# Optimization experiments

Measured on AMD Instinct MI355X. Metric: run time of the kernel, lower is better.

The kernel has to match this reference:

```python
import jax, jax.numpy as jnp
import numpy as np

B, N, C = 4, 4096, 256
NUM_HEADS = 8
NUM_GROUPS = 4  # num_groups2, recursive_index=True path
HEAD_DIM = C // NUM_HEADS
SCALE = HEAD_DIM ** -0.5


def setup_inputs() -> dict:
    key = jax.random.key(0)
    k_x, k_idx, k_qkv, k_proj, k_pb = jax.random.split(key, 5)
    x = jax.random.normal(k_x, (B, N, C), dtype=jnp.float32)
    idx = jax.random.permutation(k_idx, N)  # random token shuffle (torch.randperm)
    # nn.Linear params (torch convention: y = x @ W.T + b)
    w_qkv = jax.random.normal(k_qkv, (3 * C, C), dtype=jnp.float32) * (1.0 / np.sqrt(C))
    w_proj = jax.random.normal(k_proj, (C, C), dtype=jnp.float32) * (1.0 / np.sqrt(C))
    b_proj = jax.random.normal(k_pb, (C,), dtype=jnp.float32) * 0.01
    return {"x": x, "idx": idx, "w_qkv": w_qkv, "w_proj": w_proj, "b_proj": b_proj}


def reference(x, idx, w_qkv, w_proj, b_proj):
    g, H, d = NUM_GROUPS, NUM_HEADS, HEAD_DIM
    n = N // g  # tokens per group
    inverse = jnp.argsort(idx)
    xp = x[:, idx, :]  # shuffled tokens [B, N, C]
    # qkv projection then split into groups/heads: [B, g, n, 3, H, d]
    qkv = (xp @ w_qkv.T).reshape(B, g, n, 3, H, d)
    q = qkv[:, :, :, 0].transpose(0, 1, 3, 2, 4)  # [B, g, H, n, d]
    k = qkv[:, :, :, 1].transpose(0, 1, 3, 2, 4)
    v = qkv[:, :, :, 2].transpose(0, 1, 3, 2, 4)
    attn = jnp.einsum('bghnd,bghmd->bghnm', q, k) * SCALE  # [B, g, H, n, n]
    attn = jax.nn.softmax(attn, axis=-1)
    o = jnp.einsum('bghnm,bghmd->bghnd', attn, v)
    # [B, g, H, n, d] -> [B, g, n, H, d] -> [B, N, C] (group-major token order)
    o = o.transpose(0, 1, 3, 2, 4).reshape(B, N, C)
    o = o[:, inverse, :]  # undo the shuffle
    return o @ w_proj.T + b_proj
```

## Files before the change

### kernel.cpp

```cpp
#include <hip/hip_runtime.h>
#include <hip/hip_bf16.h>


typedef __attribute__((ext_vector_type(8))) short bf16x8;
typedef __attribute__((ext_vector_type(4))) float f32x4;

__device__ __forceinline__ unsigned short f2bf(float x){
  __hip_bfloat16 h = __float2bfloat16(x);
  return __builtin_bit_cast(unsigned short, h);
}

__device__ __forceinline__ bf16x8 cvt8(const float4 f0, const float4 f1){
  bf16x8 v;
  v[0]=(short)f2bf(f0.x); v[1]=(short)f2bf(f0.y);
  v[2]=(short)f2bf(f0.z); v[3]=(short)f2bf(f0.w);
  v[4]=(short)f2bf(f1.x); v[5]=(short)f2bf(f1.y);
  v[6]=(short)f2bf(f1.z); v[7]=(short)f2bf(f1.w);
  return v;
}

#define QSCALE (0.17677669529663687f * 1.4426950408889634f)


__global__ __launch_bounds__(256, 3) void qkv_gemm(
    const float* __restrict__ x, const int* __restrict__ idx,
    const float* __restrict__ w_qkv,
    unsigned short* __restrict__ Qb, unsigned short* __restrict__ KF,
    unsigned short* __restrict__ VF)
{
  __shared__ __align__(16) unsigned short Asl[128*64];
  __shared__ __align__(16) unsigned short Bsl[128*64];
  const int tid = threadIdx.x;
  const int bid = blockIdx.x;
  const int u   = bid >> 3, xl = bid & 7;
  const int bx  = ((u & 15) << 3) + xl;
  const int by  = u >> 4;
  const int m0 = bx << 7;
  const int bb = bx >> 5;
  const int gg = (bx >> 3) & 3;
  const int j0 = (bx & 31) << 7;
  const int n0 = by << 7;

  int srow[2], brow[2], wb[2];
  #pragma unroll
  for (int it = 0; it < 2; ++it){
    int c = (it << 8) + tid;
    int row = c >> 2;
    int k8 = (c & 3) << 3;
    srow[it] = (bb << 12) + idx[j0 + row];
    brow[it] = n0 + row;
    wb[it] = ((row << 7) + (k8 << 1)) ^ ((row & 7) << 4);
  }

  #pragma unroll
  for (int it = 0; it < 2; ++it){
    int k8 = (((it << 8) + tid) & 3) << 3;
    const float* xs = x + srow[it]*256 + k8;
    const float* wsp = w_qkv + brow[it]*256 + k8;
    *(bf16x8*)((char*)Asl + wb[it]) = cvt8(*(const float4*)(xs), *(const float4*)(xs+4));
    *(bf16x8*)((char*)Bsl + wb[it]) = cvt8(*(const float4*)(wsp), *(const float4*)(wsp+4));
  }
  __syncthreads();

  const int lane = tid & 63;
  const int w = tid >> 6, wr = w >> 1, wc = w & 1;
  const int lr = lane & 15, lg = lane >> 4;
  const int ka = lg << 3;

  f32x4 acc[4][4];
  #pragma unroll
  for (int il = 0; il < 4; ++il)
    #pragma unroll
    for (int jl = 0; jl < 4; ++jl)
      acc[il][jl] = (f32x4){0.f,0.f,0.f,0.f};

  for (int st = 0; st < 8; ++st){
    float4 a0[2], a1[2], c0[2], c1[2];
    const bool pf = (st < 7);
    if (pf){
      int kb = (st + 1) << 5;
      #pragma unroll
      for (int it = 0; it < 2; ++it){
        int k8 = (((it << 8) + tid) & 3) << 3;
        const float* xs = x + srow[it]*256 + kb + k8;
        const float* wsp = w_qkv + brow[it]*256 + kb + k8;
        a0[it] = *(const float4*)(xs);  a1[it] = *(const float4*)(xs + 4);
        c0[it] = *(const float4*)(wsp); c1[it] = *(const float4*)(wsp + 4);
      }
    }

    bf16x8 af[4], bfr[4];
    #pragma unroll
    for (int il = 0; il < 4; ++il){
      int rowA = (wr << 6) + (il << 4) + lr;
      af[il] = *(const bf16x8*)((const char*)Asl + (((rowA << 7) + (ka << 1)) ^ ((rowA & 7) << 4)));
      int rowB = (wc << 6) + (il << 4) + lr;
      bfr[il] = *(const bf16x8*)((const char*)Bsl + (((rowB << 7) + (ka << 1)) ^ ((rowB & 7) << 4)));
    }
    __builtin_amdgcn_s_setprio(1);
    #pragma unroll
    for (int il = 0; il < 4; ++il)
      #pragma unroll
      for (int jl = 0; jl < 4; ++jl)
        acc[il][jl] = __builtin_amdgcn_mfma_f32_16x16x32_bf16(af[il], bfr[jl], acc[il][jl], 0, 0, 0);
    __builtin_amdgcn_s_setprio(0);

    __syncthreads();
    if (pf){
      #pragma unroll
      for (int it = 0; it < 2; ++it){
        *(bf16x8*)((char*)Asl + wb[it]) = cvt8(a0[it], a1[it]);
        *(bf16x8*)((char*)Bsl + wb[it]) = cvt8(c0[it], c1[it]);
      }
      __syncthreads();
    }
  }

  const int s = by >> 1;
  const int hbase = ((bb << 2) + gg) << 3;
  #pragma unroll
  for (int il = 0; il < 4; ++il){
    int mr0 = m0 + (wr << 6) + (il << 4) + (lg << 2);
    int nl0 = mr0 & 1023;
    int t   = nl0 >> 5;
    #pragma unroll
    for (int jl = 0; jl < 4; ++jl){
      int ocol = ((by & 1) << 7) + (wc << 6) + (jl << 4) + lr;
      int h  = ocol >> 5, dd = ocol & 31;
      int head = hbase + h;
      if (s == 2){
        int m = nl0 & 31;
        int lane2 = ((m >> 3) << 4) + (dd & 15);
        int half = dd >> 4;
        ushort4 pk;
        pk.x = f2bf(acc[il][jl][0]); pk.y = f2bf(acc[il][jl][1]);
        pk.z = f2bf(acc[il][jl][2]); pk.w = f2bf(acc[il][jl][3]);
        *(ushort4*)(VF + head*32768 + t*1024 + half*512 + lane2*8 + (m & 7)) = pk;
      } else if (s == 1){
        int r0 = nl0 & 31;
        int f  = (r0 >> 2) & 1;
        unsigned short* dst = KF + head*32768 + t*1024 + f*512
                             + ((((dd >> 3) << 4) + ((r0 >> 3) << 2)) << 3) + (dd & 7);
        dst[0]  = f2bf(acc[il][jl][0]);
        dst[8]  = f2bf(acc[il][jl][1]);
        dst[16] = f2bf(acc[il][jl][2]);
        dst[24] = f2bf(acc[il][jl][3]);
      } else {
        unsigned short* dst = Qb + head*32768 + dd;
        #pragma unroll
        for (int q = 0; q < 4; ++q)
          dst[(nl0 + q) << 5] = f2bf(acc[il][jl][q] * QSCALE);
      }
    }
  }
}

__device__ __forceinline__ void softmax16(
    const f32x4 s0, const f32x4 s1, const f32x4 s2, const f32x4 s3,
    bf16x8& pf0, bf16x8& pf1)
{
  float p0=__builtin_amdgcn_exp2f(s0[0]);  float p1=__builtin_amdgcn_exp2f(s0[1]);
  float p2=__builtin_amdgcn_exp2f(s0[2]);  float p3=__builtin_amdgcn_exp2f(s0[3]);
  float p4=__builtin_amdgcn_exp2f(s1[0]);  float p5=__builtin_amdgcn_exp2f(s1[1]);
  float p6=__builtin_amdgcn_exp2f(s1[2]);  float p7=__builtin_amdgcn_exp2f(s1[3]);
  float p8=__builtin_amdgcn_exp2f(s2[0]);  float p9=__builtin_amdgcn_exp2f(s2[1]);
  float p10=__builtin_amdgcn_exp2f(s2[2]); float p11=__builtin_amdgcn_exp2f(s2[3]);
  float p12=__builtin_amdgcn_exp2f(s3[0]); float p13=__builtin_amdgcn_exp2f(s3[1]);
  float p14=__builtin_amdgcn_exp2f(s3[2]); float p15=__builtin_amdgcn_exp2f(s3[3]);

  pf0[0]=(short)f2bf(p0);  pf0[1]=(short)f2bf(p1);
  pf0[2]=(short)f2bf(p2);  pf0[3]=(short)f2bf(p3);
  pf0[4]=(short)f2bf(p4);  pf0[5]=(short)f2bf(p5);
  pf0[6]=(short)f2bf(p6);  pf0[7]=(short)f2bf(p7);
  pf1[0]=(short)f2bf(p8);  pf1[1]=(short)f2bf(p9);
  pf1[2]=(short)f2bf(p10); pf1[3]=(short)f2bf(p11);
  pf1[4]=(short)f2bf(p12); pf1[5]=(short)f2bf(p13);
  pf1[6]=(short)f2bf(p14); pf1[7]=(short)f2bf(p15);
}

__global__ __launch_bounds__(256, 2) void attn_kernel(
    const unsigned short* __restrict__ Qb, const unsigned short* __restrict__ KF,
    const unsigned short* __restrict__ VF, unsigned short* __restrict__ OB)
{
  __shared__ __align__(16) char lds[32768];
  const int tid  = threadIdx.x;
  const int bid  = blockIdx.x;
  const int b    = ((bid & 7) << 6) + (bid >> 3);
  const int head = b >> 2;
  const int qblk = b & 3;
  const int lane = tid & 63;
  const int w  = tid >> 6;
  const int lr = lane & 15, lg = lane >> 4;
  const int q0 = qblk * 256 + w * 64;

  const unsigned short* kf = KF + head*32768;
  const unsigned short* vf = VF + head*32768;
  const unsigned short* qbase = Qb + head*32768;

  {
    bf16x8 k0 = *(const bf16x8*)(kf + tid*8);
    bf16x8 k1 = *(const bf16x8*)(kf + 2048 + tid*8);
    bf16x8 v0 = *(const bf16x8*)(vf + tid*8);
    bf16x8 v1 = *(const bf16x8*)(vf + 2048 + tid*8);
    *(bf16x8*)(lds + tid*16)          = k0;
    *(bf16x8*)(lds + 4096 + tid*16)   = k1;
    *(bf16x8*)(lds + 8192 + tid*16)   = v0;
    *(bf16x8*)(lds + 12288 + tid*16)  = v1;
  }

  bf16x8 qf[4];
  #pragma unroll
  for (int g = 0; g < 4; ++g)
    qf[g] = *(const bf16x8*)(qbase + (q0 + g*16 + lr)*32 + (lg << 3));

  const short one_bf = (short)0x3F80;
  bf16x8 onesf = {one_bf,one_bf,one_bf,one_bf,one_bf,one_bf,one_bf,one_bf};

  f32x4 o0[4], o1[4], ls[4];
  #pragma unroll
  for (int g = 0; g < 4; ++g){
    o0[g] = (f32x4){0.f,0.f,0.f,0.f};
    o1[g] = (f32x4){0.f,0.f,0.f,0.f};
    ls[g] = (f32x4){0.f,0.f,0.f,0.f};
  }
  const f32x4 zz={0.f,0.f,0.f,0.f};

  __syncthreads();
  int cur = 0;
  for (int it = 0; it < 8; ++it){
    bf16x8 kr0, kr1, vr0, vr1;
    const bool pfch = (it < 7);
    if (pfch){
      const unsigned short* kg = kf + (it+1)*4096 + tid*8;
      const unsigned short* vg = vf + (it+1)*4096 + tid*8;
      kr0 = *(const bf16x8*)(kg);
      kr1 = *(const bf16x8*)(kg + 2048);
      vr0 = *(const bf16x8*)(vg);
      vr1 = *(const bf16x8*)(vg + 2048);
    }

    const char* KL = lds + cur*16384 + lane*16;
    const char* VL = KL + 8192;
    #pragma unroll
    for (int hh = 0; hh < 2; ++hh){
      const char* kp_ = KL + hh*4096;
      const char* vp_ = VL + hh*4096;
      bf16x8 kA0 = *(const bf16x8*)(kp_);
      bf16x8 kB0 = *(const bf16x8*)(kp_ + 1024);
      bf16x8 kA1 = *(const bf16x8*)(kp_ + 2048);
      bf16x8 kB1 = *(const bf16x8*)(kp_ + 3072);
      bf16x8 v00 = *(const bf16x8*)(vp_);
      bf16x8 v01 = *(const bf16x8*)(vp_ + 1024);
      bf16x8 v10 = *(const bf16x8*)(vp_ + 2048);
      bf16x8 v11 = *(const bf16x8*)(vp_ + 3072);

      __builtin_amdgcn_s_setprio(1);
      f32x4 sA0 = __builtin_amdgcn_mfma_f32_16x16x32_bf16(kA0, qf[0], zz, 0, 0, 0);
      f32x4 sB0 = __builtin_amdgcn_mfma_f32_16x16x32_bf16(kB0, qf[0], zz, 0, 0, 0);
      f32x4 sA1 = __builtin_amdgcn_mfma_f32_16x16x32_bf16(kA1, qf[0], zz, 0, 0, 0);
      f32x4 sB1 = __builtin_amdgcn_mfma_f32_16x16x32_bf16(kB1, qf[0], zz, 0, 0, 0);
      __builtin_amdgcn_s_setprio(0);

      #pragma unroll
      for (int g = 0; g < 4; ++g){
        f32x4 nA0, nB0, nA1, nB1;
        if (g < 3){
          __builtin_amdgcn_s_setprio(1);
          nA0 = __builtin_amdgcn_mfma_f32_16x16x32_bf16(kA0, qf[g+1], zz, 0, 0, 0);
          nB0 = __builtin_amdgcn_mfma_f32_16x16x32_bf16(kB0, qf[g+1], zz, 0, 0, 0);
          nA1 = __builtin_amdgcn_mfma_f32_16x16x32_bf16(kA1, qf[g+1], zz, 0, 0, 0);
          nB1 = __builtin_amdgcn_mfma_f32_16x16x32_bf16(kB1, qf[g+1], zz, 0, 0, 0);
          __builtin_amdgcn_s_setprio(0);
        }
        bf16x8 pf0, pf1;
        softmax16(sA0, sB0, sA1, sB1, pf0, pf1);
        __builtin_amdgcn_s_setprio(1);
        o0[g] = __builtin_amdgcn_mfma_f32_16x16x32_bf16(pf0, v00, o0[g], 0, 0, 0);
        o1[g] = __builtin_amdgcn_mfma_f32_16x16x32_bf16(pf0, v01, o1[g], 0, 0, 0);
        o0[g] = __builtin_amdgcn_mfma_f32_16x16x32_bf16(pf1, v10, o0[g], 0, 0, 0);
        o1[g] = __builtin_amdgcn_mfma_f32_16x16x32_bf16(pf1, v11, o1[g], 0, 0, 0);
        ls[g] = __builtin_amdgcn_mfma_f32_16x16x32_bf16(pf0, onesf, ls[g], 0, 0, 0);
        ls[g] = __builtin_amdgcn_mfma_f32_16x16x32_bf16(pf1, onesf, ls[g], 0, 0, 0);
        __builtin_amdgcn_s_setprio(0);
        if (g < 3){ sA0 = nA0; sB0 = nB0; sA1 = nA1; sB1 = nB1; }
      }
    }

    if (pfch){
      char* db = lds + (cur^1)*16384;
      *(bf16x8*)(db + tid*16)          = kr0;
      *(bf16x8*)(db + 4096 + tid*16)   = kr1;
      *(bf16x8*)(db + 8192 + tid*16)   = vr0;
      *(bf16x8*)(db + 12288 + tid*16)  = vr1;
    }
    __syncthreads();
    cur ^= 1;
  }

  const int bI = head >> 5, gI = (head >> 3) & 3, hI = head & 7;
  unsigned short* obase = OB + (bI*4096 + gI*1024 + q0)*256 + hI*32;
  #pragma unroll
  for (int g = 0; g < 4; ++g){
    #pragma unroll
    for (int q = 0; q < 4; ++q){
      float iv = 1.0f / ls[g][q];
      int r = (g << 4) + (lg << 2) + q;
      obase[r*256 + lr]      = f2bf(o0[g][q] * iv);
      obase[r*256 + 16 + lr] = f2bf(o1[g][q] * iv);
    }
  }
}

__global__ __launch_bounds__(256) void proj_gemm(
    const unsigned short* __restrict__ OB, const float* __restrict__ w_proj,
    const float* __restrict__ b_proj, const int* __restrict__ idx,
    float* __restrict__ out)
{
  __shared__ unsigned short Alds[64*256];
  __shared__ unsigned short Blds[64*256];
  const int tid = threadIdx.x;
  const int m0 = blockIdx.x << 6;
  const int bb = m0 >> 12;

  #pragma unroll
  for (int it = 0; it < 8; ++it){
    int c = (it << 8) + tid;
    int row = c >> 5;
    int k8 = (c & 31) << 3;
    int byt = ((row << 9) + (k8 << 1)) ^ ((row & 7) << 4);
    *(bf16x8*)((char*)Alds + byt) = *(const bf16x8*)(OB + (m0+row)*256 + k8);
  }

  const int w  = tid >> 6, lane = tid & 63;
  const int lr = lane & 15, lg = lane >> 4;
  const int wr = w >> 1,  wc = w & 1;

  for (int nt = 0; nt < 2; ++nt){
    const int n0 = blockIdx.y * 128 + nt * 64;
    __syncthreads();
    #pragma unroll
    for (int it = 0; it < 8; ++it){
      int c = (it << 8) + tid;
      int row = c >> 5;
      int k8 = (c & 31) << 3;
      const float4 f0 = *(const float4*)(w_proj + (n0+row)*256 + k8);
      const float4 f1 = *(const float4*)(w_proj + (n0+row)*256 + k8 + 4);
      bf16x8 v;
      v[0]=(short)f2bf(f0.x); v[1]=(short)f2bf(f0.y);
      v[2]=(short)f2bf(f0.z); v[3]=(short)f2bf(f0.w);
      v[4]=(short)f2bf(f1.x); v[5]=(short)f2bf(f1.y);
      v[6]=(short)f2bf(f1.z); v[7]=(short)f2bf(f1.w);
      int byt = ((row << 9) + (k8 << 1)) ^ ((row & 7) << 4);
      *(bf16x8*)((char*)Blds + byt) = v;
    }
    __syncthreads();

    f32x4 acc[2][2];
    #pragma unroll
    for (int i=0;i<2;++i)
      #pragma unroll
      for (int j=0;j<2;++j)
        acc[i][j] = (f32x4){0.f,0.f,0.f,0.f};

    #pragma unroll
    for (int ks = 0; ks < 8; ++ks){
      bf16x8 af[2], bfr[2];
      int ka = (ks << 5) + (lg << 3);
      #pragma unroll
      for (int i=0;i<2;++i){
        int rowA = (wr << 5) + (i << 4) + lr;
        int bytA = ((rowA << 9) + (ka << 1)) ^ ((rowA & 7) << 4);
        af[i] = *(const bf16x8*)((const char*)Alds + bytA);
        int rowB = (wc << 5) + (i << 4) + lr;
        int bytB = ((rowB << 9) + (ka << 1)) ^ ((rowB & 7) << 4);
        bfr[i] = *(const bf16x8*)((const char*)Blds + bytB);
      }
      #pragma unroll
      for (int i=0;i<2;++i)
        #pragma unroll
        for (int j=0;j<2;++j)
          acc[i][j] = __builtin_amdgcn_mfma_f32_16x16x32_bf16(af[i], bfr[j], acc[i][j], 0, 0, 0);
    }

    #pragma unroll
    for (int i=0;i<2;++i){
      int mr0 = m0 + (wr << 5) + (i << 4) + (lg << 2);
      int rd[4];
      #pragma unroll
      for (int q=0;q<4;++q)
        rd[q] = (bb << 12) + idx[(mr0 + q) & 4095];
      #pragma unroll
      for (int j=0;j<2;++j){
        int o = n0 + (wc << 5) + (j << 4) + lr;
        float bias = b_proj[o];
        #pragma unroll
        for (int q=0;q<4;++q)
          out[rd[q]*256 + o] = acc[i][j][q] + bias;
      }
    }
  }
}

extern "C" void kernel_launch(void* const* d_in, const int* in_sizes, int n_in,
                              void* d_out, int out_size, void* d_ws, size_t ws_size,
                              hipStream_t stream)
{
  const float* x      = (const float*)d_in[0];
  const int*   idx    = (const int*)  d_in[1];
  const float* w_qkv  = (const float*)d_in[2];
  const float* w_proj = (const float*)d_in[3];
  const float* b_proj = (const float*)d_in[4];
  float* out = (float*)d_out;

  char* ws = (char*)d_ws;
  unsigned short* Qb = (unsigned short*)(ws);
  unsigned short* KF = (unsigned short*)(ws + (8u  << 20));
  unsigned short* VF = (unsigned short*)(ws + (16u << 20));
  unsigned short* OB = (unsigned short*)(ws + (24u << 20));

  qkv_gemm<<<dim3(768), 256, 0, stream>>>(x, idx, w_qkv, Qb, KF, VF);
  attn_kernel<<<dim3(512), 256, 0, stream>>>(Qb, KF, VF, OB);
  proj_gemm<<<dim3(256, 2), 256, 0, stream>>>(OB, w_proj, b_proj, idx, out);
}
```

Before: 56.24 us.

## Split attention over key halves and combine partial results in separate kernel

```diff
diff --git a/kernel.cpp b/kernel.cpp
--- a/kernel.cpp
+++ b/kernel.cpp
@@ -178,23 +178,26 @@
   pf1[6]=(short)f2bf(p14); pf1[7]=(short)f2bf(p15);
 }
 
-__global__ __launch_bounds__(256, 2) void attn_kernel(
+__global__ __launch_bounds__(256, 3) void attn_half(
     const unsigned short* __restrict__ Qb, const unsigned short* __restrict__ KF,
-    const unsigned short* __restrict__ VF, unsigned short* __restrict__ OB)
+    const unsigned short* __restrict__ VF, float* __restrict__ OP,
+    float* __restrict__ LS)
 {
   __shared__ __align__(16) char lds[32768];
   const int tid  = threadIdx.x;
   const int bid  = blockIdx.x;
-  const int b    = ((bid & 7) << 6) + (bid >> 3);
-  const int head = b >> 2;
-  const int qblk = b & 3;
+  const int b    = ((bid & 7) << 7) + (bid >> 3);
+  const int head = b >> 3;
+  const int sub  = b & 7;
+  const int qblk = sub >> 1;
+  const int mh   = sub & 1;
   const int lane = tid & 63;
   const int w  = tid >> 6;
   const int lr = lane & 15, lg = lane >> 4;
   const int q0 = qblk * 256 + w * 64;
 
-  const unsigned short* kf = KF + head*32768;
-  const unsigned short* vf = VF + head*32768;
+  const unsigned short* kf = KF + head*32768 + (mh << 14);
+  const unsigned short* vf = VF + head*32768 + (mh << 14);
   const unsigned short* qbase = Qb + head*32768;
 
   {
@@ -227,9 +230,9 @@
 
   __syncthreads();
   int cur = 0;
-  for (int it = 0; it < 8; ++it){
+  for (int it = 0; it < 4; ++it){
     bf16x8 kr0, kr1, vr0, vr1;
-    const bool pfch = (it < 7);
+    const bool pfch = (it < 3);
     if (pfch){
       const unsigned short* kg = kf + (it+1)*4096 + tid*8;
       const unsigned short* vg = vf + (it+1)*4096 + tid*8;
@@ -298,17 +301,46 @@
   }
 
   const int bI = head >> 5, gI = (head >> 3) & 3, hI = head & 7;
-  unsigned short* obase = OB + (bI*4096 + gI*1024 + q0)*256 + hI*32;
+  const int rbase = bI*4096 + gI*1024 + q0;
+  float* opb = OP + (size_t)mh*4194304 + (size_t)rbase*256 + hI*32;
   #pragma unroll
   for (int g = 0; g < 4; ++g){
     #pragma unroll
     for (int q = 0; q < 4; ++q){
-      float iv = 1.0f / ls[g][q];
       int r = (g << 4) + (lg << 2) + q;
-      obase[r*256 + lr]      = f2bf(o0[g][q] * iv);
-      obase[r*256 + 16 + lr] = f2bf(o1[g][q] * iv);
-    }
-  }
+      opb[r*256 + lr]      = o0[g][q];
+      opb[r*256 + 16 + lr] = o1[g][q];
+    }
+  }
+  if (lr == 0){
+    float* lsb = LS + ((size_t)(mh*16384 + rbase) << 3) + hI;
+    #pragma unroll
+    for (int g = 0; g < 4; ++g)
+      #pragma unroll
+      for (int q = 0; q < 4; ++q)
+        lsb[((g << 4) + (lg << 2) + q) << 3] = ls[g][q];
+  }
+}
+
+__global__ __launch_bounds__(256) void combine_halves(
+    const float* __restrict__ OP, const float* __restrict__ LS,
+    unsigned short* __restrict__ OB)
+{
+  int gid = blockIdx.x*256 + threadIdx.x;
+  int e0 = gid << 3;
+  int row = e0 >> 8;
+  int hI  = (e0 & 255) >> 5;
+  float inv = 1.0f / (LS[(row << 3) + hI] + LS[((16384 + row) << 3) + hI]);
+  const float4 a0 = *(const float4*)(OP + e0);
+  const float4 a1 = *(const float4*)(OP + e0 + 4);
+  const float4 b0 = *(const float4*)(OP + 4194304 + e0);
+  const float4 b1 = *(const float4*)(OP + 4194304 + e0 + 4);
+  bf16x8 v;
+  v[0]=(short)f2bf((a0.x+b0.x)*inv); v[1]=(short)f2bf((a0.y+b0.y)*inv);
+  v[2]=(short)f2bf((a0.z+b0.z)*inv); v[3]=(short)f2bf((a0.w+b0.w)*inv);
+  v[4]=(short)f2bf((a1.x+b1.x)*inv); v[5]=(short)f2bf((a1.y+b1.y)*inv);
+  v[6]=(short)f2bf((a1.z+b1.z)*inv); v[7]=(short)f2bf((a1.w+b1.w)*inv);
+  *(bf16x8*)(OB + e0) = v;
 }
 
 __global__ __launch_bounds__(256) void proj_gemm(
@@ -417,8 +449,11 @@
   unsigned short* KF = (unsigned short*)(ws + (8u  << 20));
   unsigned short* VF = (unsigned short*)(ws + (16u << 20));
   unsigned short* OB = (unsigned short*)(ws + (24u << 20));
+  float*          OP = (float*)        (ws + (32u << 20));
+  float*          LSb= (float*)        (ws + (64u << 20));
 
   qkv_gemm<<<dim3(768), 256, 0, stream>>>(x, idx, w_qkv, Qb, KF, VF);
-  attn_kernel<<<dim3(512), 256, 0, stream>>>(Qb, KF, VF, OB);
+  attn_half<<<dim3(1024), 256, 0, stream>>>(Qb, KF, VF, OP, LSb);
+  combine_halves<<<dim3(2048), 256, 0, stream>>>(OP, LSb, OB);
   proj_gemm<<<dim3(256, 2), 256, 0, stream>>>(OB, w_proj, b_proj, idx, out);
 }
```

Result: slower. 65.19 us (+15.9%).
